# Kernel tuning notes

Measured on AMD Instinct MI355X. Metric: run time of the kernel, lower is better.

Reference implementation:

```python
import jax, jax.numpy as jnp
import numpy as np

B, N, C = 8, 1024, 768
H = 12
HD = C // H  # 64
SCALE = HD ** -0.5


def setup_inputs() -> dict:
    key = jax.random.key(0)
    k1, k2, k3, k4 = jax.random.split(key, 4)
    x = jax.random.normal(k1, (B, N, C), dtype=jnp.float32)
    # torch Linear weights are [out, in]; qkv has no bias (qkv_bias=False)
    w_qkv = jax.random.normal(k2, (3 * C, C), dtype=jnp.float32) * (C ** -0.5)
    w_proj = jax.random.normal(k3, (C, C), dtype=jnp.float32) * (C ** -0.5)
    b_proj = jax.random.normal(k4, (C,), dtype=jnp.float32) * 0.01
    return {"x": x, "w_qkv": w_qkv, "w_proj": w_proj, "b_proj": b_proj}


def reference(x, w_qkv, w_proj, b_proj):
    b, n, c = x.shape
    # qkv: [B, N, 3C] -> [3, B, H, N, HD]
    qkv = (x @ w_qkv.T).reshape(b, n, 3, H, c // H).transpose(2, 0, 3, 1, 4)
    q, k, v = qkv[0], qkv[1], qkv[2]
    attn = jnp.einsum('bhqd,bhkd->bhqk', q, k) * SCALE
    attn = jax.nn.softmax(attn, axis=-1)
    out = jnp.einsum('bhqk,bhkd->bhqd', attn, v)          # [B, H, N, HD]
    out = out.transpose(0, 2, 1, 3).reshape(b, n, c)      # [B, N, C]
    out = out @ w_proj.T + b_proj
    return out
```

## Files before the change

### kernel.cpp

```cpp
#include <hip/hip_runtime.h>
#include <hip/hip_bf16.h>
#include <cstdint>

#define TB 8
#define TN 1024
#define TC 768
#define TH 12
#define THD 64
#define TM (TB*TN)
#define TNQKV (3*TC)
#define QSCALE_LOG2E 0.18033688011112042f
#define THR_BITS 11.541560327111708f

typedef __attribute__((ext_vector_type(8))) short s16x8;
typedef __attribute__((ext_vector_type(4))) float f32x4;
typedef __attribute__((ext_vector_type(16))) float f32x16;
typedef __attribute__((ext_vector_type(2))) unsigned int u32x2;

__device__ __forceinline__ unsigned short f2bf(float f) {
    union { float f; unsigned int u; } v; v.f = f;
    unsigned int u = v.u;
    return (unsigned short)((u + 0x7FFFu + ((u >> 16) & 1u)) >> 16);
}

__device__ __forceinline__ float bf2f(unsigned short h) {
    union { float f; unsigned int u; } v; v.u = ((unsigned int)h) << 16;
    return v.f;
}

__device__ __forceinline__ unsigned int cvt_pk_bf16(float lo, float hi) {
    unsigned int r;
    asm("v_cvt_pk_bf16_f32 %0, %1, %2" : "=v"(r) : "v"(lo), "v"(hi));
    return r;
}

__device__ __forceinline__ void gload_lds16(const unsigned short* g, unsigned short* l) {
    __builtin_amdgcn_global_load_lds(
        (const __attribute__((address_space(1))) unsigned int*)g,
        (__attribute__((address_space(3))) unsigned int*)l,
        16, 0, 0);
}

__global__ __launch_bounds__(256) void cvt3_kernel(
    const float* __restrict__ a, unsigned short* __restrict__ oa, int na,
    const float* __restrict__ b, unsigned short* __restrict__ ob, int nb,
    const float* __restrict__ c, unsigned short* __restrict__ oc, int nc)
{
    int i = blockIdx.x * blockDim.x + threadIdx.x;
    const float* src; unsigned short* dst; int idx;
    if (i < na)           { src = a; dst = oa; idx = i; }
    else if (i < na + nb) { src = b; dst = ob; idx = i - na; }
    else if (i < na + nb + nc) { src = c; dst = oc; idx = i - na - nb; }
    else return;
    f32x4 x0 = *(const f32x4*)(src + (size_t)idx * 8);
    f32x4 x1 = *(const f32x4*)(src + (size_t)idx * 8 + 4);
    s16x8 r;
    #pragma unroll
    for (int e = 0; e < 4; e++) r[e] = (short)f2bf(x0[e]);
    #pragma unroll
    for (int e = 0; e < 4; e++) r[4 + e] = (short)f2bf(x1[e]);
    *(s16x8*)(dst + (size_t)idx * 8) = r;
}

template<bool BIAS, bool OBF16, bool VSPLIT>
__global__ __launch_bounds__(256) void gemm_bt(
    const unsigned short* __restrict__ A,
    const unsigned short* __restrict__ Bm,
    void* __restrict__ Cout,
    const float* __restrict__ bias,
    unsigned short* __restrict__ vt,
    int M, int Nn, int K)
{
    __shared__ unsigned short As[128 * 64];
    __shared__ unsigned short Bs[128 * 64];
    const int t = threadIdx.x;
    const int w = t >> 6, l = t & 63;
    const int wm = w >> 1, wn = w & 1;
    const int bm = blockIdx.x, bn = blockIdx.y;
    const int l31 = l & 31, khi = l >> 5;
    const int r7 = l31 & 7;

    f32x16 acc00 = {}, acc01 = {}, acc10 = {}, acc11 = {};

    const unsigned short* Ab = A + (size_t)bm * 128 * K;
    const unsigned short* Bb = Bm + (size_t)bn * 128 * K;

    for (int kt = 0; kt < K; kt += 64) {
        __syncthreads();
        #pragma unroll
        for (int j = 0; j < 4; j++) {
            const int s = j * 256 + t, row = s >> 3, c = s & 7;
            const int g = c ^ (row & 7);
            gload_lds16(Ab + (size_t)row * K + kt + g * 8, As + s * 8);
            gload_lds16(Bb + (size_t)row * K + kt + g * 8, Bs + s * 8);
        }
        __syncthreads();
        #pragma unroll
        for (int ks = 0; ks < 4; ks++) {
            const int ch = ((ks << 1) + khi) ^ r7;
            const unsigned short* Ar = As + (wm * 64 + l31) * 64 + ch * 8;
            const unsigned short* Br = Bs + (wn * 64 + l31) * 64 + ch * 8;
            s16x8 a0 = *(const s16x8*)(Ar);
            s16x8 a1 = *(const s16x8*)(Ar + 32 * 64);
            s16x8 b0 = *(const s16x8*)(Br);
            s16x8 b1 = *(const s16x8*)(Br + 32 * 64);
            acc00 = __builtin_amdgcn_mfma_f32_32x32x16_bf16(a0, b0, acc00, 0, 0, 0);
            acc01 = __builtin_amdgcn_mfma_f32_32x32x16_bf16(a0, b1, acc01, 0, 0, 0);
            acc10 = __builtin_amdgcn_mfma_f32_32x32x16_bf16(a1, b0, acc10, 0, 0, 0);
            acc11 = __builtin_amdgcn_mfma_f32_32x32x16_bf16(a1, b1, acc11, 0, 0, 0);
        }
    }

    const int r0 = bm * 128 + wm * 64;
    const int c0 = bn * 128 + wn * 64;
    f32x16 accs[2][2] = {{acc00, acc01}, {acc10, acc11}};
    if constexpr (VSPLIT) {
        if (bn >= 12) {
            const int bb = (r0 >> 10) * TH;
            #pragma unroll
            for (int X = 0; X < 2; X++)
                #pragma unroll
                for (int Y = 0; Y < 2; Y++) {
                    const int dg = c0 + Y * 32 + l31 - 2 * TC;
                    unsigned short* vp = vt + ((size_t)(bb + (dg >> 6)) << 16)
                                            + (dg & 63) * TN;
                    const int k0 = (r0 & 1023) + X * 32 + 4 * khi;
                    #pragma unroll
                    for (int g = 0; g < 4; g++) {
                        u32x2 r;
                        r[0] = cvt_pk_bf16(accs[X][Y][g * 4], accs[X][Y][g * 4 + 1]);
                        r[1] = cvt_pk_bf16(accs[X][Y][g * 4 + 2], accs[X][Y][g * 4 + 3]);
                        *(u32x2*)(vp + k0 + 8 * g) = r;
                    }
                }
            return;
        }
    }
    if constexpr (OBF16) {
        unsigned short* O = (unsigned short*)Cout;
        #pragma unroll
        for (int X = 0; X < 2; X++)
            #pragma unroll
            for (int Y = 0; Y < 2; Y++) {
                const int cc = c0 + Y * 32 + l31;
                const int rb = r0 + X * 32 + 4 * khi;
                #pragma unroll
                for (int i = 0; i < 16; i++)
                    O[(size_t)(rb + (i & 3) + 8 * (i >> 2)) * Nn + cc] =
                        f2bf(accs[X][Y][i]);
            }
    } else {
        float* O = (float*)Cout;
        #pragma unroll
        for (int X = 0; X < 2; X++)
            #pragma unroll
            for (int Y = 0; Y < 2; Y++) {
                const int cc = c0 + Y * 32 + l31;
                const int rb = r0 + X * 32 + 4 * khi;
                float bv = 0.f;
                if constexpr (BIAS) bv = bias[cc];
                #pragma unroll
                for (int i = 0; i < 16; i++)
                    O[(size_t)(rb + (i & 3) + 8 * (i >> 2)) * Nn + cc] =
                        accs[X][Y][i] + bv;
            }
    }
}

__global__ __launch_bounds__(512) void attn_kernel(
    const unsigned short* __restrict__ qkv,
    const unsigned short* __restrict__ vt,
    unsigned short* __restrict__ out)
{
    const int bid = blockIdx.x;
    const int vid = (bid & 7) * 96 + (bid >> 3);
    const int bh = vid >> 3;
    const int qt = vid & 7;
    const int b = bh / TH, h = bh % TH;
    const int t = threadIdx.x, w = t >> 6, l = t & 63;
    const int lr = l & 15, lh = l >> 4;
    const int qbase = qt * 128 + w * 16;

    __shared__ unsigned short Kbuf[2][64 * 64];
    __shared__ unsigned short Vbuf[2][64 * 64];
    __shared__ unsigned short plds[8][16 * 64];

    const unsigned short* kbase = qkv + (size_t)(b * TN) * TNQKV + TC + h * THD;
    const unsigned short* vtb = vt + (size_t)bh * THD * TN;

    const int srow_lo = (l >> 3);
    const int schunk = (l & 7) ^ srow_lo;
    const int srow = w * 8 + srow_lo;
    const int sdst = w * 512 + l * 8;

    const unsigned short* qptr = qkv + (size_t)(b * TN + qbase + lr) * TNQKV + h * THD;
    s16x8 bq[2];
    #pragma unroll
    for (int cj = 0; cj < 2; cj++) {
        s16x8 raw = *(const s16x8*)(qptr + cj * 32 + lh * 8);
        #pragma unroll
        for (int e = 0; e < 8; e++)
            bq[cj][e] = (short)f2bf(bf2f((unsigned short)raw[e]) * QSCALE_LOG2E);
    }
    s16x8 av1;
    #pragma unroll
    for (int e = 0; e < 8; e++) av1[e] = (short)0x3F80;

    f32x4 o[5] = {};
    float m2 = -1e30f;
    unsigned short* pw = plds[w];
    const int lr7 = lr & 7;

    gload_lds16(kbase + (size_t)srow * TNQKV + schunk * 8, &Kbuf[0][sdst]);
    gload_lds16(vtb + (size_t)srow * TN + schunk * 8, &Vbuf[0][sdst]);
    __syncthreads();

    for (int it = 0; it < 16; it++) {
        const int kt = it * 64;
        const int cur = it & 1, nxt = cur ^ 1;
        if (it + 1 < 16) {
            const int ktn = kt + 64;
            gload_lds16(kbase + (size_t)(ktn + srow) * TNQKV + schunk * 8, &Kbuf[nxt][sdst]);
            gload_lds16(vtb + (size_t)srow * TN + ktn + schunk * 8, &Vbuf[nxt][sdst]);
        }
        const unsigned short* Kc = Kbuf[cur];
        const unsigned short* Vc = Vbuf[cur];

        f32x4 s[4];
        __builtin_amdgcn_s_setprio(1);
        #pragma unroll
        for (int kk = 0; kk < 4; kk++) {
            const int r = kk * 16 + lr;
            s16x8 ak0 = *(const s16x8*)(Kc + r * 64 + ((lh ^ lr7) * 8));
            s16x8 ak1 = *(const s16x8*)(Kc + r * 64 + (((4 + lh) ^ lr7) * 8));
            f32x4 z = {0.f, 0.f, 0.f, 0.f};
            z = __builtin_amdgcn_mfma_f32_16x16x32_bf16(ak0, bq[0], z, 0, 0, 0);
            z = __builtin_amdgcn_mfma_f32_16x16x32_bf16(ak1, bq[1], z, 0, 0, 0);
            s[kk] = z;
        }
        __builtin_amdgcn_s_setprio(0);

        float v[16];
        #pragma unroll
        for (int kk = 0; kk < 4; kk++)
            #pragma unroll
            for (int i = 0; i < 4; i++) v[kk * 4 + i] = s[kk][i];
        float mx = fmaxf(fmaxf(v[0], v[1]), v[2]);
        #pragma unroll
        for (int j = 3; j + 1 < 16; j += 2) mx = fmaxf(fmaxf(mx, v[j]), v[j + 1]);
        mx = fmaxf(mx, v[15]);
        if (!__all(mx <= m2 + THR_BITS)) {
            float rmx = fmaxf(mx, __shfl_xor(mx, 16, 64));
            rmx = fmaxf(rmx, __shfl_xor(rmx, 32, 64));
            float newm = fmaxf(m2, rmx);
            float corr = __builtin_amdgcn_exp2f(m2 - newm);
            m2 = newm;
            #pragma unroll
            for (int nd = 0; nd < 5; nd++)
                #pragma unroll
                for (int i = 0; i < 4; i++) o[nd][i] *= corr;
        }
        #pragma unroll
        for (int kk = 0; kk < 4; kk++)
            #pragma unroll
            for (int i = 0; i < 4; i++)
                s[kk][i] = __builtin_amdgcn_exp2f(s[kk][i] - m2);

        #pragma unroll
        for (int kk = 0; kk < 4; kk++) {
            u32x2 pk;
            pk[0] = cvt_pk_bf16(s[kk][0], s[kk][1]);
            pk[1] = cvt_pk_bf16(s[kk][2], s[kk][3]);
            const int wch = ((kk << 1) + (lh >> 1)) ^ lr7;
            *(u32x2*)(pw + lr * 64 + wch * 8 + (lh & 1) * 4) = pk;
        }
        __builtin_amdgcn_s_setprio(1);
        #pragma unroll
        for (int ktile = 0; ktile < 2; ktile++) {
            const int rch = ((ktile << 2) + lh) ^ lr7;
            s16x8 bp = *(const s16x8*)(pw + lr * 64 + rch * 8);
            #pragma unroll
            for (int nd = 0; nd < 4; nd++) {
                const int d = nd * 16 + lr;
                s16x8 av = *(const s16x8*)(
                    Vc + d * 64 + ((((ktile << 2) + lh) ^ lr7) * 8));
                o[nd] = __builtin_amdgcn_mfma_f32_16x16x32_bf16(av, bp, o[nd], 0, 0, 0);
            }
            o[4] = __builtin_amdgcn_mfma_f32_16x16x32_bf16(av1, bp, o[4], 0, 0, 0);
        }
        __builtin_amdgcn_s_setprio(0);
        __syncthreads();
    }

    float inv = 1.f / o[4][0];
    unsigned short* op = out + (size_t)(b * TN + qbase + lr) * TC + h * THD;
    #pragma unroll
    for (int nd = 0; nd < 4; nd++) {
        u32x2 r;
        r[0] = cvt_pk_bf16(o[nd][0] * inv, o[nd][1] * inv);
        r[1] = cvt_pk_bf16(o[nd][2] * inv, o[nd][3] * inv);
        *(u32x2*)(op + nd * 16 + lh * 4) = r;
    }
}

extern "C" void kernel_launch(void* const* d_in, const int* in_sizes, int n_in,
                              void* d_out, int out_size, void* d_ws, size_t ws_size,
                              hipStream_t stream) {
    const float* x      = (const float*)d_in[0];
    const float* w_qkv  = (const float*)d_in[1];
    const float* w_proj = (const float*)d_in[2];
    const float* b_proj = (const float*)d_in[3];
    float* out = (float*)d_out;

    unsigned short* xb   = (unsigned short*)d_ws;
    unsigned short* wqb  = xb   + (size_t)TM * TC;
    unsigned short* wpb  = wqb  + (size_t)TNQKV * TC;
    unsigned short* qkvb = wpb  + (size_t)TC * TC;
    unsigned short* vtb  = qkvb + (size_t)TM * TNQKV;
    unsigned short* aob  = vtb  + (size_t)TB * TH * THD * TN;

    const int na = TM * TC / 8, nb = TNQKV * TC / 8, nc = TC * TC / 8;
    cvt3_kernel<<<(na + nb + nc + 255) / 256, 256, 0, stream>>>(
        x, xb, na, w_qkv, wqb, nb, w_proj, wpb, nc);

    gemm_bt<false, true, true><<<dim3(TM / 128, TNQKV / 128), 256, 0, stream>>>(
        xb, wqb, (void*)qkvb, nullptr, vtb, TM, TNQKV, TC);

    attn_kernel<<<768, 512, 0, stream>>>(qkvb, vtb, aob);

    gemm_bt<true, false, false><<<dim3(TM / 128, TC / 128), 256, 0, stream>>>(
        aob, wpb, (void*)out, b_proj, nullptr, TM, TC, TC);
}
```

Baseline: 111.8 us.

## Double-buffer LDS tiles in GEMM to overlap global loads with MFMA

The GEMM kernel now keeps two LDS buffers for A and B. It issues the direct-to-LDS global loads for the next K tile before computing on the current one, and uses vmcnt waits so the memory latency overlaps with MFMA work. This doubles LDS use to 64KB per block, which may reduce occupancy. It also depends on the vmcnt(8) count exactly matching the eight loads issued per stage.

```diff
diff --git a/kernel.cpp b/kernel.cpp
--- a/kernel.cpp
+++ b/kernel.cpp
@@ -71,8 +71,8 @@
     unsigned short* __restrict__ vt,
     int M, int Nn, int K)
 {
-    __shared__ unsigned short As[128 * 64];
-    __shared__ unsigned short Bs[128 * 64];
+    __shared__ unsigned short As[2][128 * 64];
+    __shared__ unsigned short Bs[2][128 * 64];
     const int t = threadIdx.x;
     const int w = t >> 6, l = t & 63;
     const int wm = w >> 1, wn = w & 1;
@@ -85,21 +85,37 @@
     const unsigned short* Ab = A + (size_t)bm * 128 * K;
     const unsigned short* Bb = Bm + (size_t)bn * 128 * K;
 
-    for (int kt = 0; kt < K; kt += 64) {
-        __syncthreads();
+    auto stage = [&](int bufi, int kt) {
         #pragma unroll
         for (int j = 0; j < 4; j++) {
             const int s = j * 256 + t, row = s >> 3, c = s & 7;
             const int g = c ^ (row & 7);
-            gload_lds16(Ab + (size_t)row * K + kt + g * 8, As + s * 8);
-            gload_lds16(Bb + (size_t)row * K + kt + g * 8, Bs + s * 8);
-        }
-        __syncthreads();
+            gload_lds16(Ab + (size_t)row * K + kt + g * 8, &As[bufi][s * 8]);
+            gload_lds16(Bb + (size_t)row * K + kt + g * 8, &Bs[bufi][s * 8]);
+        }
+    };
+
+    stage(0, 0);
+    asm volatile("s_waitcnt vmcnt(0)" ::: "memory");
+    __builtin_amdgcn_s_barrier();
+
+    const int nkt = K / 64;
+    for (int it = 0; it < nkt; it++) {
+        const int cur = it & 1, nxt = cur ^ 1;
+        if (it + 1 < nkt) {
+            stage(nxt, (it + 1) * 64);
+            asm volatile("s_waitcnt vmcnt(8)" ::: "memory");
+        } else {
+            asm volatile("s_waitcnt vmcnt(0)" ::: "memory");
+        }
+        __builtin_amdgcn_s_barrier();
+        const unsigned short* Ac = As[cur];
+        const unsigned short* Bc = Bs[cur];
         #pragma unroll
         for (int ks = 0; ks < 4; ks++) {
             const int ch = ((ks << 1) + khi) ^ r7;
-            const unsigned short* Ar = As + (wm * 64 + l31) * 64 + ch * 8;
-            const unsigned short* Br = Bs + (wn * 64 + l31) * 64 + ch * 8;
+            const unsigned short* Ar = Ac + (wm * 64 + l31) * 64 + ch * 8;
+            const unsigned short* Br = Bc + (wn * 64 + l31) * 64 + ch * 8;
             s16x8 a0 = *(const s16x8*)(Ar);
             s16x8 a1 = *(const s16x8*)(Ar + 32 * 64);
             s16x8 b0 = *(const s16x8*)(Br);
@@ -109,6 +125,7 @@
             acc10 = __builtin_amdgcn_mfma_f32_32x32x16_bf16(a1, b0, acc10, 0, 0, 0);
             acc11 = __builtin_amdgcn_mfma_f32_32x32x16_bf16(a1, b1, acc11, 0, 0, 0);
         }
+        __builtin_amdgcn_s_barrier();
     }
 
     const int r0 = bm * 128 + wm * 64;
```

After: 118.3 us. 1.06x slower.
